# Optimization experiments

Measured on AMD Instinct MI355X. Metric: run time of the kernel, lower is better.

## Reference

```python
import jax, jax.numpy as jnp
import numpy as np

N_NODES = 100000
N_EDGES = 3200000


def _gcn_conv(x, src, dst, W, b, n):
    # symmetric GCN normalization with self-loops (PyG GCNConv default)
    deg = jax.ops.segment_sum(jnp.ones_like(dst, dtype=x.dtype), dst, num_segments=n)
    dinv = jnp.where(deg > 0, jax.lax.rsqrt(jnp.maximum(deg, 1e-12)), 0.0)
    norm = dinv[src] * dinv[dst]                       # [E+N]
    h = x @ W                                          # [n, out]
    msg = h[src] * norm[:, None]                       # gather + scale
    out = jax.ops.segment_sum(msg, dst, num_segments=n)  # scatter-add
    return out + b


def setup_inputs() -> dict:
    key = jax.random.key(0)
    k1, k2, k3, k4 = jax.random.split(key, 4)
    feat = jax.random.normal(k1, (N_NODES, 1), dtype=jnp.float32)
    edge_ix = jax.random.randint(k2, (2, N_EDGES), 0, N_NODES, dtype=jnp.int64)
    W1 = jax.random.normal(k3, (1, 32), dtype=jnp.float32) * (1.0 / 1.0)
    b1 = jnp.zeros((32,), dtype=jnp.float32)
    W2 = jax.random.normal(k4, (32, 64), dtype=jnp.float32) * (1.0 / np.sqrt(32.0))
    b2 = jnp.zeros((64,), dtype=jnp.float32)
    return {"feat": feat, "edge_ix": edge_ix, "W1": W1, "b1": b1, "W2": W2, "b2": b2}


def reference(feat, edge_ix, W1, b1, W2, b2):
    n = feat.shape[0]
    # add self loops once; reuse for both layers
    loops = jnp.arange(n, dtype=edge_ix.dtype)
    src = jnp.concatenate([edge_ix[0], loops])
    dst = jnp.concatenate([edge_ix[1], loops])
    x = jax.nn.relu(_gcn_conv(feat, src, dst, W1, b1, n))
    x = jax.nn.relu(_gcn_conv(x, src, dst, W2, b2, n))
    return x
```

## Files before the change

kernel.cpp:

```cpp
#include <hip/hip_runtime.h>


#define TPB 256
#define TPBW 1024
#define NSBMAX 1024
#define SBSZ 256
#define LBITS 8
#define SPLIT 4
#define NCHUNK 256

__global__ void k_init(const int* __restrict__ e32, int E, int* __restrict__ flag,
                       const float* __restrict__ W1, const float* __restrict__ b1,
                       const float* __restrict__ W2, float* __restrict__ upm,
                       int* __restrict__ bzero) {
    __shared__ int ok;
    __shared__ float sw[32], sb[32];
    int t = threadIdx.x;
    if (t == 0) ok = 1;
    if (t < 32) { sw[t] = W1[t]; sb[t] = b1[t]; }
    __syncthreads();
    int stride = E / 2048; if (stride < 1) stride = 1;
    bool bad = false;
#pragma unroll
    for (int i = 0; i < 8; ++i) {
        long k = (long)(t * 8 + i) * stride + 1;
        if (k < E && e32[2 * k + 1] != 0) bad = true;
    }
    if (bad) atomicAnd(&ok, 0);
    if (t < 64) {
        float up = 0.f, um = 0.f;
#pragma unroll
        for (int c = 0; c < 32; ++c) {
            float w = sw[c];
            float w2 = W2[c * 64 + t];
            up = fmaf(fmaxf(w, 0.f), w2, up);
            um = fmaf(fmaxf(-w, 0.f), w2, um);
        }
        upm[t] = up;
        upm[64 + t] = um;
    }
    __syncthreads();
    if (t == 0) {
        *flag = ok;
        int z = 1;
        for (int c = 0; c < 32; ++c) if (sb[c] != 0.f) z = 0;
        *bzero = z;
    }
}

__global__ void k_hist2(const int* __restrict__ e32, const int* __restrict__ flag,
                        int E, int NSB, int chunk, int* __restrict__ H) {
    __shared__ int sh[NSBMAX];
    int c = blockIdx.x;
    int c0 = c * chunk;
    int c1 = c0 + chunk; if (c1 > E) c1 = E;
    for (int i = threadIdx.x; i < NSB; i += TPBW) sh[i] = 0;
    __syncthreads();
    int f = *flag;
    for (int e = c0 + threadIdx.x; e < c1; e += TPBW) {
        int d = e32[((long)E + e) << f];
        atomicAdd(&sh[d >> LBITS], 1);
    }
    __syncthreads();
    for (int i = threadIdx.x; i < NSB; i += TPBW) H[(size_t)c * NSB + i] = sh[i];
}

__global__ void k_colscan(const int* __restrict__ H, int NSB,
                          int* __restrict__ P2, int* __restrict__ colsum) {
    __shared__ int s[NCHUNK];
    int b = blockIdx.x, t = threadIdx.x;
    int v = H[(size_t)t * NSB + b];
    s[t] = v;
    __syncthreads();
    for (int off = 1; off < NCHUNK; off <<= 1) {
        int x = s[t];
        int u = (t >= off) ? s[t - off] : 0;
        __syncthreads();
        s[t] = x + u;
        __syncthreads();
    }
    P2[(size_t)t * NSB + b] = s[t] - v;
    if (t == NCHUNK - 1) colsum[b] = s[t];
}

__global__ void k_scan(const int* __restrict__ colsum, int NSB, int E,
                       int* __restrict__ base) {
    __shared__ int s[TPB];
    int K = (NSB + TPB - 1) / TPB;
    int t = threadIdx.x;
    int i0 = t * K;
    int tot = 0;
    for (int k = 0; k < K; ++k) { int i = i0 + k; if (i < NSB) tot += colsum[i]; }
    s[t] = tot;
    __syncthreads();
    for (int off = 1; off < TPB; off <<= 1) {
        int v = s[t];
        int u = (t >= off) ? s[t - off] : 0;
        __syncthreads();
        s[t] = v + u;
        __syncthreads();
    }
    int run = s[t] - tot;
    for (int k = 0; k < K; ++k) {
        int i = i0 + k;
        if (i < NSB) { base[i] = run; run += colsum[i]; }
    }
    if (t == 0) base[NSB] = E;
}

__global__ void k_part2(const int* __restrict__ e32, const int* __restrict__ flag,
                        int E, int NSB, const int* __restrict__ base,
                        const int* __restrict__ P2, unsigned int* __restrict__ P,
                        int chunk) {
    __shared__ int sh[NSBMAX];
    int c = blockIdx.x;
    int c0 = c * chunk;
    int c1 = c0 + chunk; if (c1 > E) c1 = E;
    for (int i = threadIdx.x; i < NSB; i += TPBW)
        sh[i] = base[i] + P2[(size_t)c * NSB + i];
    __syncthreads();
    int f = *flag;
    int sshift = 32 - LBITS;
    for (int e = c0 + threadIdx.x; e < c1; e += TPBW) {
        long ee = (long)e << f;
        int s = e32[ee];
        int d = e32[(((long)E) << f) + ee];
        int b = d >> LBITS;
        int pos = atomicAdd(&sh[b], 1);
        P[pos] = (unsigned)s | ((unsigned)(d & (SBSZ - 1)) << sshift);
    }
}

__global__ void k_degS(const unsigned int* __restrict__ P, const int* __restrict__ base,
                       int n, int* __restrict__ cntP) {
    __shared__ int cnt[SBSZ];
    int bb = blockIdx.x / SPLIT, pp = blockIdx.x % SPLIT;
    int t = threadIdx.x;
    cnt[t] = 0;
    __syncthreads();
    int p0 = base[bb], len = base[bb + 1] - p0;
    int s0 = p0 + (int)((long)len * pp / SPLIT);
    int s1 = p0 + (int)((long)len * (pp + 1) / SPLIT);
    int sshift = 32 - LBITS;
    for (int p = s0 + t; p < s1; p += TPB)
        atomicAdd(&cnt[P[p] >> sshift], 1);
    __syncthreads();
    int v = (bb << LBITS) + t;
    if (v < n) cntP[pp * n + v] = cnt[t];
}

__global__ void k_prep1(const int* __restrict__ cntP, const float* __restrict__ feat,
                        int n, float* __restrict__ dinv, float* __restrict__ g) {
    int v = blockIdx.x * TPB + threadIdx.x;
    if (v >= n) return;
    int c = 0;
#pragma unroll
    for (int pp = 0; pp < SPLIT; ++pp) c += cntP[pp * n + v];
    float di = rsqrtf((float)(c + 1));
    dinv[v] = di;
    g[v] = di * feat[v];
}

__global__ void k_aggAS(const unsigned int* __restrict__ P, const int* __restrict__ base,
                        int n, const float* __restrict__ g, float* __restrict__ AP) {
    __shared__ float A[SBSZ];
    int bb = blockIdx.x / SPLIT, pp = blockIdx.x % SPLIT;
    int t = threadIdx.x;
    A[t] = 0.f;
    __syncthreads();
    int p0 = base[bb], len = base[bb + 1] - p0;
    int s0 = p0 + (int)((long)len * pp / SPLIT);
    int s1 = p0 + (int)((long)len * (pp + 1) / SPLIT);
    int sshift = 32 - LBITS;
    unsigned smask = (1u << sshift) - 1;
    for (int p = s0 + t; p < s1; p += TPB) {
        unsigned e = P[p];
        atomicAdd(&A[e >> sshift], g[e & smask]);
    }
    __syncthreads();
    int v = (bb << LBITS) + t;
    if (v < n) AP[pp * n + v] = A[t];
}

__global__ void k_prep2(const float* __restrict__ AP, const float* __restrict__ g,
                        const float* __restrict__ dinv, int n, const int* __restrict__ bzero,
                        float* __restrict__ qs, float2* __restrict__ pd,
                        float* __restrict__ Yagg) {
    int v = blockIdx.x * TPB + threadIdx.x;
    if (v >= n) return;
    float A = g[v];
#pragma unroll
    for (int pp = 0; pp < SPLIT; ++pp) A += AP[pp * n + v];
    float di = dinv[v];
    float px = di * A;
    qs[v] = di * px;
    if (!*bzero) {
        pd[v] = make_float2(px, di);
        float4* Y = (float4*)(Yagg + (size_t)v * 32);
#pragma unroll
        for (int i = 0; i < 8; ++i) Y[i] = make_float4(0.f, 0.f, 0.f, 0.f);
    }
}

__global__ void k_aggTS(const unsigned int* __restrict__ P, const int* __restrict__ base,
                        int n, const float* __restrict__ qs, float2* __restrict__ SP2) {
    __shared__ float Sp[SBSZ], Sm[SBSZ];
    int bb = blockIdx.x / SPLIT, pp = blockIdx.x % SPLIT;
    int t = threadIdx.x;
    Sp[t] = 0.f; Sm[t] = 0.f;
    __syncthreads();
    int p0 = base[bb], len = base[bb + 1] - p0;
    int s0 = p0 + (int)((long)len * pp / SPLIT);
    int s1 = p0 + (int)((long)len * (pp + 1) / SPLIT);
    int sshift = 32 - LBITS;
    unsigned smask = (1u << sshift) - 1;
    for (int p = s0 + t; p < s1; p += TPB) {
        unsigned e = P[p];
        float q = qs[e & smask];
        int l = e >> sshift;
        float* addr = (q >= 0.f) ? &Sp[l] : &Sm[l];
        atomicAdd(addr, fabsf(q));
    }
    __syncthreads();
    int v = (bb << LBITS) + t;
    if (v < n) SP2[pp * n + v] = make_float2(Sp[t], Sm[t]);
}

__global__ void k_out(const float* __restrict__ qs, const float* __restrict__ dinv,
                      const float2* __restrict__ SP2, const float* __restrict__ upm,
                      const float* __restrict__ b2, const int* __restrict__ bzero,
                      int n, float* __restrict__ out) {
    if (!*bzero) return;
    __shared__ float su[192];
    if (threadIdx.x < 192) su[threadIdx.x] = (threadIdx.x < 128) ? upm[threadIdx.x] : b2[threadIdx.x - 128];
    __syncthreads();
    int o = blockIdx.x * TPB + threadIdx.x;
    if (o >= n * 64) return;
    int v = o >> 6, k = o & 63;
    float qv = qs[v];
    float Sp = fmaxf(qv, 0.f), Sm = fmaxf(-qv, 0.f);
#pragma unroll
    for (int pp = 0; pp < SPLIT; ++pp) { float2 s = SP2[pp * n + v]; Sp += s.x; Sm += s.y; }
    float r = fmaf(dinv[v], fmaf(Sp, su[k], Sm * su[64 + k]), su[128 + k]);
    out[o] = fmaxf(r, 0.f);
}

__global__ void k_aggY(const int* __restrict__ e32, const int* __restrict__ flag,
                       int E, const int* __restrict__ bzero,
                       const float2* __restrict__ pd,
                       const float* __restrict__ W1, const float* __restrict__ b1,
                       float* __restrict__ Yagg) {
    if (*bzero) return;
    __shared__ float sw[32], sb[32];
    if (threadIdx.x < 32) { sw[threadIdx.x] = W1[threadIdx.x]; sb[threadIdx.x] = b1[threadIdx.x]; }
    __syncthreads();
    int sh = *flag;
    long stride = (long)gridDim.x * TPB;
    for (long e = (long)blockIdx.x * TPB + threadIdx.x; e < E; e += stride) {
        int s = e32[e << sh];
        int d = e32[((long)E + e) << sh];
        float2 p = pd[s];
#pragma unroll
        for (int c = 0; c < 32; ++c) {
            float y = p.y * fmaxf(fmaf(sw[c], p.x, sb[c] * p.y), 0.f);
            atomicAdd(&Yagg[(size_t)d * 32 + c], y);
        }
    }
}

__global__ void k_final_gen(const float2* __restrict__ pd, const float* __restrict__ Yagg,
                            const float* __restrict__ W1, const float* __restrict__ b1,
                            const float* __restrict__ W2, const float* __restrict__ b2,
                            const int* __restrict__ bzero, int n, float* __restrict__ out) {
    if (*bzero) return;
    __shared__ float sW[32 * 64];
    __shared__ float sb2[64];
    __shared__ float sagg[8][33];
    int t = threadIdx.x;
    for (int i = t; i < 32 * 64; i += TPB) sW[i] = W2[i];
    if (t < 64) sb2[t] = b2[t];
    int vl = t >> 5, c = t & 31;
    int nblk = (n + 7) / 8;
    for (int blk = blockIdx.x; blk < nblk; blk += gridDim.x) {
        int v = blk * 8 + vl;
        float a = 0.f;
        if (v < n) {
            float2 p = pd[v];
            float dv = p.y;
            float yv = fmaxf(fmaf(W1[c], p.x, b1[c] * p.y), 0.f);
            a = dv * (dv * yv + Yagg[(size_t)v * 32 + c]);
        }
        __syncthreads();
        sagg[vl][c] = a;
        __syncthreads();
        if (v < n) {
            float o0 = sb2[c], o1 = sb2[c + 32];
#pragma unroll
            for (int j = 0; j < 32; ++j) {
                float x = sagg[vl][j];
                o0 += x * sW[j * 64 + c];
                o1 += x * sW[j * 64 + 32 + c];
            }
            out[(size_t)v * 64 + c]      = fmaxf(o0, 0.f);
            out[(size_t)v * 64 + 32 + c] = fmaxf(o1, 0.f);
        }
    }
}

static inline size_t align256(size_t x) { return (x + 255) & ~(size_t)255; }

extern "C" void kernel_launch(void* const* d_in, const int* in_sizes, int n_in,
                              void* d_out, int out_size, void* d_ws, size_t ws_size,
                              hipStream_t stream) {
    const float* feat = (const float*)d_in[0];
    const int*   e32  = (const int*)d_in[1];
    const float* W1   = (const float*)d_in[2];
    const float* b1   = (const float*)d_in[3];
    const float* W2   = (const float*)d_in[4];
    const float* b2   = (const float*)d_in[5];
    float* out = (float*)d_out;

    int n = in_sizes[0];
    int E = in_sizes[1] / 2;

    int NSB = (n + SBSZ - 1) >> LBITS;

    char* w = (char*)d_ws;
    size_t off = 0;
    auto alloc = [&](size_t bytes) -> char* { char* p = w + off; off = align256(off + bytes); return p; };
    unsigned int* P = (unsigned int*)alloc((size_t)E * 4);
    int*    H     = (int*)alloc((size_t)NCHUNK * NSB * 4);
    int*    P2    = (int*)alloc((size_t)NCHUNK * NSB * 4);
    int*    colsum= (int*)alloc((size_t)NSB * 4);
    int*    base  = (int*)alloc((size_t)(NSB + 1) * 4);
    int*    cntP  = (int*)alloc((size_t)SPLIT * n * 4);
    float*  AP    = (float*)alloc((size_t)SPLIT * n * 4);
    float2* SP2   = (float2*)alloc((size_t)SPLIT * n * 8);
    float*  dinv  = (float*)alloc((size_t)n * 4);
    float*  g     = (float*)alloc((size_t)n * 4);
    float*  qs    = (float*)alloc((size_t)n * 4);
    float2* pd    = (float2*)alloc((size_t)n * 8);
    float*  upm   = (float*)alloc(128 * 4);
    int*    flag  = (int*)alloc(4);
    int*    bzero = (int*)alloc(4);
    float*  Yagg  = (float*)alloc((size_t)n * 32 * 4);

    int chunk = (E + NCHUNK - 1) / NCHUNK;
    int gN = (n + TPB - 1) / TPB;
    int gS = NSB * SPLIT;
    int gO = (n * 64 + TPB - 1) / TPB;

    hipLaunchKernelGGL(k_init,      dim3(1),      dim3(TPB),  0, stream, e32, E, flag, W1, b1, W2, upm, bzero);
    hipLaunchKernelGGL(k_hist2,     dim3(NCHUNK), dim3(TPBW), 0, stream, e32, flag, E, NSB, chunk, H);
    hipLaunchKernelGGL(k_colscan,   dim3(NSB),    dim3(NCHUNK), 0, stream, H, NSB, P2, colsum);
    hipLaunchKernelGGL(k_scan,      dim3(1),      dim3(TPB),  0, stream, colsum, NSB, E, base);
    hipLaunchKernelGGL(k_part2,     dim3(NCHUNK), dim3(TPBW), 0, stream, e32, flag, E, NSB, base, P2, P, chunk);
    hipLaunchKernelGGL(k_degS,      dim3(gS),     dim3(TPB),  0, stream, P, base, n, cntP);
    hipLaunchKernelGGL(k_prep1,     dim3(gN),     dim3(TPB),  0, stream, cntP, feat, n, dinv, g);
    hipLaunchKernelGGL(k_aggAS,     dim3(gS),     dim3(TPB),  0, stream, P, base, n, g, AP);
    hipLaunchKernelGGL(k_prep2,     dim3(gN),     dim3(TPB),  0, stream, AP, g, dinv, n, bzero, qs, pd, Yagg);
    hipLaunchKernelGGL(k_aggTS,     dim3(gS),     dim3(TPB),  0, stream, P, base, n, qs, SP2);
    hipLaunchKernelGGL(k_out,       dim3(gO),     dim3(TPB),  0, stream, qs, dinv, SP2, upm, b2, bzero, n, out);
    hipLaunchKernelGGL(k_aggY,      dim3(512),    dim3(TPB),  0, stream, e32, flag, E, bzero, pd, W1, b1, Yagg);
    hipLaunchKernelGGL(k_final_gen, dim3(1024),   dim3(TPB),  0, stream, pd, Yagg, W1, b1, W2, b2, bzero, n, out);
}
```

Baseline: 122.4 us.

## Fuse scan and per-node prep kernels via last-block counters, vectorize edge loads

```diff
diff --git a/kernel.cpp b/kernel.cpp
--- a/kernel.cpp
+++ b/kernel.cpp
@@ -12,12 +12,13 @@
 __global__ void k_init(const int* __restrict__ e32, int E, int* __restrict__ flag,
                        const float* __restrict__ W1, const float* __restrict__ b1,
                        const float* __restrict__ W2, float* __restrict__ upm,
-                       int* __restrict__ bzero) {
+                       int* __restrict__ bzero, int* __restrict__ ctrs, int nctr) {
     __shared__ int ok;
     __shared__ float sw[32], sb[32];
     int t = threadIdx.x;
     if (t == 0) ok = 1;
     if (t < 32) { sw[t] = W1[t]; sb[t] = b1[t]; }
+    for (int i = t; i < nctr; i += TPB) ctrs[i] = 0;
     __syncthreads();
     int stride = E / 2048; if (stride < 1) stride = 1;
     bool bad = false;
@@ -57,17 +58,38 @@
     for (int i = threadIdx.x; i < NSB; i += TPBW) sh[i] = 0;
     __syncthreads();
     int f = *flag;
-    for (int e = c0 + threadIdx.x; e < c1; e += TPBW) {
-        int d = e32[((long)E + e) << f];
-        atomicAdd(&sh[d >> LBITS], 1);
+    if (((E | c0) & 1) == 0) {
+        if (f) {
+            const int4* d4 = (const int4*)e32;
+            for (int e = c0 + threadIdx.x * 2; e < c1; e += TPBW * 2) {
+                int4 dd = d4[(E + e) >> 1];
+                atomicAdd(&sh[dd.x >> LBITS], 1);
+                if (e + 1 < c1) atomicAdd(&sh[dd.z >> LBITS], 1);
+            }
+        } else {
+            const int2* d2 = (const int2*)e32;
+            for (int e = c0 + threadIdx.x * 2; e < c1; e += TPBW * 2) {
+                int2 dd = d2[(E + e) >> 1];
+                atomicAdd(&sh[dd.x >> LBITS], 1);
+                if (e + 1 < c1) atomicAdd(&sh[dd.y >> LBITS], 1);
+            }
+        }
+    } else {
+        for (int e = c0 + threadIdx.x; e < c1; e += TPBW) {
+            int d = e32[((long)E + e) << f];
+            atomicAdd(&sh[d >> LBITS], 1);
+        }
     }
     __syncthreads();
     for (int i = threadIdx.x; i < NSB; i += TPBW) H[(size_t)c * NSB + i] = sh[i];
 }
 
-__global__ void k_colscan(const int* __restrict__ H, int NSB,
-                          int* __restrict__ P2, int* __restrict__ colsum) {
+__global__ void k_colscan(const int* __restrict__ H, int NSB, int E,
+                          int* __restrict__ P2, int* __restrict__ colsum,
+                          int* __restrict__ base, int* __restrict__ ctr) {
     __shared__ int s[NCHUNK];
+    __shared__ int s2a[TPB];
+    __shared__ int lastf;
     int b = blockIdx.x, t = threadIdx.x;
     int v = H[(size_t)t * NSB + b];
     s[t] = v;
@@ -81,26 +103,25 @@
     }
     P2[(size_t)t * NSB + b] = s[t] - v;
     if (t == NCHUNK - 1) colsum[b] = s[t];
-}
-
-__global__ void k_scan(const int* __restrict__ colsum, int NSB, int E,
-                       int* __restrict__ base) {
-    __shared__ int s[TPB];
+    __syncthreads();
+    if (t == 0) { __threadfence(); lastf = (atomicAdd(ctr, 1) == gridDim.x - 1); }
+    __syncthreads();
+    if (!lastf) return;
+    __threadfence();
     int K = (NSB + TPB - 1) / TPB;
-    int t = threadIdx.x;
     int i0 = t * K;
     int tot = 0;
     for (int k = 0; k < K; ++k) { int i = i0 + k; if (i < NSB) tot += colsum[i]; }
-    s[t] = tot;
+    s2a[t] = tot;
     __syncthreads();
     for (int off = 1; off < TPB; off <<= 1) {
-        int v = s[t];
-        int u = (t >= off) ? s[t - off] : 0;
-        __syncthreads();
-        s[t] = v + u;
-        __syncthreads();
-    }
-    int run = s[t] - tot;
+        int x = s2a[t];
+        int u = (t >= off) ? s2a[t - off] : 0;
+        __syncthreads();
+        s2a[t] = x + u;
+        __syncthreads();
+    }
+    int run = s2a[t] - tot;
     for (int k = 0; k < K; ++k) {
         int i = i0 + k;
         if (i < NSB) { base[i] = run; run += colsum[i]; }
@@ -121,20 +142,55 @@
     __syncthreads();
     int f = *flag;
     int sshift = 32 - LBITS;
-    for (int e = c0 + threadIdx.x; e < c1; e += TPBW) {
-        long ee = (long)e << f;
-        int s = e32[ee];
-        int d = e32[(((long)E) << f) + ee];
-        int b = d >> LBITS;
-        int pos = atomicAdd(&sh[b], 1);
-        P[pos] = (unsigned)s | ((unsigned)(d & (SBSZ - 1)) << sshift);
-    }
-}
-
-__global__ void k_degS(const unsigned int* __restrict__ P, const int* __restrict__ base,
-                       int n, int* __restrict__ cntP) {
+    if (((E | c0) & 1) == 0) {
+        if (f) {
+            const int4* s4 = (const int4*)e32;
+            for (int e = c0 + threadIdx.x * 2; e < c1; e += TPBW * 2) {
+                int4 ss = s4[e >> 1];
+                int4 dd = s4[(E + e) >> 1];
+                int b0 = dd.x >> LBITS;
+                int pos0 = atomicAdd(&sh[b0], 1);
+                P[pos0] = (unsigned)ss.x | ((unsigned)(dd.x & (SBSZ - 1)) << sshift);
+                if (e + 1 < c1) {
+                    int b1i = dd.z >> LBITS;
+                    int pos1 = atomicAdd(&sh[b1i], 1);
+                    P[pos1] = (unsigned)ss.z | ((unsigned)(dd.z & (SBSZ - 1)) << sshift);
+                }
+            }
+        } else {
+            const int2* s2 = (const int2*)e32;
+            for (int e = c0 + threadIdx.x * 2; e < c1; e += TPBW * 2) {
+                int2 ss = s2[e >> 1];
+                int2 dd = s2[(E + e) >> 1];
+                int b0 = dd.x >> LBITS;
+                int pos0 = atomicAdd(&sh[b0], 1);
+                P[pos0] = (unsigned)ss.x | ((unsigned)(dd.x & (SBSZ - 1)) << sshift);
+                if (e + 1 < c1) {
+                    int b1i = dd.y >> LBITS;
+                    int pos1 = atomicAdd(&sh[b1i], 1);
+                    P[pos1] = (unsigned)ss.y | ((unsigned)(dd.y & (SBSZ - 1)) << sshift);
+                }
+            }
+        }
+    } else {
+        for (int e = c0 + threadIdx.x; e < c1; e += TPBW) {
+            long ee = (long)e << f;
+            int s = e32[ee];
+            int d = e32[(((long)E) << f) + ee];
+            int b = d >> LBITS;
+            int pos = atomicAdd(&sh[b], 1);
+            P[pos] = (unsigned)s | ((unsigned)(d & (SBSZ - 1)) << sshift);
+        }
+    }
+}
+
+__global__ void k_degSP(const unsigned int* __restrict__ P, const int* __restrict__ base,
+                        int n, const float* __restrict__ feat, int* __restrict__ cntP,
+                        float* __restrict__ dinv, float* __restrict__ g,
+                        int* __restrict__ ctrE) {
     __shared__ int cnt[SBSZ];
-    int bb = blockIdx.x / SPLIT, pp = blockIdx.x % SPLIT;
+    __shared__ int lastf;
+    int bb = blockIdx.x >> 2, pp = blockIdx.x & (SPLIT - 1);
     int t = threadIdx.x;
     cnt[t] = 0;
     __syncthreads();
@@ -147,24 +203,29 @@
     __syncthreads();
     int v = (bb << LBITS) + t;
     if (v < n) cntP[pp * n + v] = cnt[t];
-}
-
-__global__ void k_prep1(const int* __restrict__ cntP, const float* __restrict__ feat,
-                        int n, float* __restrict__ dinv, float* __restrict__ g) {
-    int v = blockIdx.x * TPB + threadIdx.x;
-    if (v >= n) return;
-    int c = 0;
-#pragma unroll
-    for (int pp = 0; pp < SPLIT; ++pp) c += cntP[pp * n + v];
-    float di = rsqrtf((float)(c + 1));
-    dinv[v] = di;
-    g[v] = di * feat[v];
-}
-
-__global__ void k_aggAS(const unsigned int* __restrict__ P, const int* __restrict__ base,
-                        int n, const float* __restrict__ g, float* __restrict__ AP) {
+    __syncthreads();
+    if (t == 0) { __threadfence(); lastf = (atomicAdd(&ctrE[bb], 1) == SPLIT - 1); }
+    __syncthreads();
+    if (!lastf) return;
+    __threadfence();
+    if (v < n) {
+        int c = 0;
+#pragma unroll
+        for (int q = 0; q < SPLIT; ++q) c += cntP[q * n + v];
+        float di = rsqrtf((float)(c + 1));
+        dinv[v] = di;
+        g[v] = di * feat[v];
+    }
+}
+
+__global__ void k_aggASP(const unsigned int* __restrict__ P, const int* __restrict__ base,
+                         int n, const float* __restrict__ g, const float* __restrict__ dinv,
+                         const int* __restrict__ bzero, float* __restrict__ AP,
+                         float* __restrict__ qs, float2* __restrict__ pd,
+                         float* __restrict__ Yagg, int* __restrict__ ctrF) {
     __shared__ float A[SBSZ];
-    int bb = blockIdx.x / SPLIT, pp = blockIdx.x % SPLIT;
+    __shared__ int lastf;
+    int bb = blockIdx.x >> 2, pp = blockIdx.x & (SPLIT - 1);
     int t = threadIdx.x;
     A[t] = 0.f;
     __syncthreads();
@@ -180,32 +241,36 @@
     __syncthreads();
     int v = (bb << LBITS) + t;
     if (v < n) AP[pp * n + v] = A[t];
-}
-
-__global__ void k_prep2(const float* __restrict__ AP, const float* __restrict__ g,
-                        const float* __restrict__ dinv, int n, const int* __restrict__ bzero,
-                        float* __restrict__ qs, float2* __restrict__ pd,
-                        float* __restrict__ Yagg) {
-    int v = blockIdx.x * TPB + threadIdx.x;
-    if (v >= n) return;
-    float A = g[v];
-#pragma unroll
-    for (int pp = 0; pp < SPLIT; ++pp) A += AP[pp * n + v];
-    float di = dinv[v];
-    float px = di * A;
-    qs[v] = di * px;
-    if (!*bzero) {
-        pd[v] = make_float2(px, di);
-        float4* Y = (float4*)(Yagg + (size_t)v * 32);
-#pragma unroll
-        for (int i = 0; i < 8; ++i) Y[i] = make_float4(0.f, 0.f, 0.f, 0.f);
-    }
-}
-
-__global__ void k_aggTS(const unsigned int* __restrict__ P, const int* __restrict__ base,
-                        int n, const float* __restrict__ qs, float2* __restrict__ SP2) {
+    __syncthreads();
+    if (t == 0) { __threadfence(); lastf = (atomicAdd(&ctrF[bb], 1) == SPLIT - 1); }
+    __syncthreads();
+    if (!lastf) return;
+    __threadfence();
+    if (v < n) {
+        float Av = g[v];
+#pragma unroll
+        for (int q = 0; q < SPLIT; ++q) Av += AP[q * n + v];
+        float di = dinv[v];
+        float px = di * Av;
+        qs[v] = di * px;
+        if (!*bzero) {
+            pd[v] = make_float2(px, di);
+            float4* Y = (float4*)(Yagg + (size_t)v * 32);
+#pragma unroll
+            for (int i = 0; i < 8; ++i) Y[i] = make_float4(0.f, 0.f, 0.f, 0.f);
+        }
+    }
+}
+
+__global__ void k_aggTSP(const unsigned int* __restrict__ P, const int* __restrict__ base,
+                         int n, const float* __restrict__ qs, const float* __restrict__ dinv,
+                         const float* __restrict__ upm, const float* __restrict__ b2,
+                         const int* __restrict__ bzero, float2* __restrict__ SP2,
+                         float* __restrict__ out, int* __restrict__ ctrG) {
     __shared__ float Sp[SBSZ], Sm[SBSZ];
-    int bb = blockIdx.x / SPLIT, pp = blockIdx.x % SPLIT;
+    __shared__ float su[192];
+    __shared__ int lastf;
+    int bb = blockIdx.x >> 2, pp = blockIdx.x & (SPLIT - 1);
     int t = threadIdx.x;
     Sp[t] = 0.f; Sm[t] = 0.f;
     __syncthreads();
@@ -222,27 +287,33 @@
         atomicAdd(addr, fabsf(q));
     }
     __syncthreads();
-    int v = (bb << LBITS) + t;
+    int v0 = bb << LBITS;
+    int v = v0 + t;
     if (v < n) SP2[pp * n + v] = make_float2(Sp[t], Sm[t]);
-}
-
-__global__ void k_out(const float* __restrict__ qs, const float* __restrict__ dinv,
-                      const float2* __restrict__ SP2, const float* __restrict__ upm,
-                      const float* __restrict__ b2, const int* __restrict__ bzero,
-                      int n, float* __restrict__ out) {
-    if (!*bzero) return;
-    __shared__ float su[192];
-    if (threadIdx.x < 192) su[threadIdx.x] = (threadIdx.x < 128) ? upm[threadIdx.x] : b2[threadIdx.x - 128];
-    __syncthreads();
-    int o = blockIdx.x * TPB + threadIdx.x;
-    if (o >= n * 64) return;
-    int v = o >> 6, k = o & 63;
-    float qv = qs[v];
-    float Sp = fmaxf(qv, 0.f), Sm = fmaxf(-qv, 0.f);
-#pragma unroll
-    for (int pp = 0; pp < SPLIT; ++pp) { float2 s = SP2[pp * n + v]; Sp += s.x; Sm += s.y; }
-    float r = fmaf(dinv[v], fmaf(Sp, su[k], Sm * su[64 + k]), su[128 + k]);
-    out[o] = fmaxf(r, 0.f);
+    __syncthreads();
+    if (t == 0) { __threadfence(); lastf = (atomicAdd(&ctrG[bb], 1) == SPLIT - 1); }
+    __syncthreads();
+    if (!lastf || !*bzero) return;
+    __threadfence();
+    if (t < 192) su[t] = (t < 192) ? ((t < 128) ? upm[t] : b2[t - 128]) : 0.f;
+    float Fp = 0.f, Fm = 0.f;
+    if (v < n) {
+        float qv = qs[v];
+        float sp = fmaxf(qv, 0.f), sm = fmaxf(-qv, 0.f);
+#pragma unroll
+        for (int q = 0; q < SPLIT; ++q) { float2 s2v = SP2[q * n + v]; sp += s2v.x; sm += s2v.y; }
+        float di = dinv[v];
+        Fp = di * sp; Fm = di * sm;
+    }
+    __syncthreads();
+    Sp[t] = Fp; Sm[t] = Fm;
+    __syncthreads();
+    int nv = n - v0; if (nv > SBSZ) nv = SBSZ; if (nv < 0) nv = 0;
+    for (int o = t; o < nv * 64; o += TPB) {
+        int vl = o >> 6, k = o & 63;
+        float r = fmaf(Sp[vl], su[k], fmaf(Sm[vl], su[64 + k], su[128 + k]));
+        out[(size_t)(v0 + vl) * 64 + k] = fmaxf(r, 0.f);
+    }
 }
 
 __global__ void k_aggY(const int* __restrict__ e32, const int* __restrict__ flag,
@@ -324,6 +395,7 @@
     int E = in_sizes[1] / 2;
 
     int NSB = (n + SBSZ - 1) >> LBITS;
+    int nctr = 1 + 3 * NSB;
 
     char* w = (char*)d_ws;
     size_t off = 0;
@@ -343,24 +415,25 @@
     float*  upm   = (float*)alloc(128 * 4);
     int*    flag  = (int*)alloc(4);
     int*    bzero = (int*)alloc(4);
+    int*    ctrs  = (int*)alloc((size_t)nctr * 4);
     float*  Yagg  = (float*)alloc((size_t)n * 32 * 4);
 
+    int* ctrC = ctrs;
+    int* ctrE = ctrs + 1;
+    int* ctrF = ctrs + 1 + NSB;
+    int* ctrG = ctrs + 1 + 2 * NSB;
+
     int chunk = (E + NCHUNK - 1) / NCHUNK;
-    int gN = (n + TPB - 1) / TPB;
+    if (chunk & 1) chunk++;
     int gS = NSB * SPLIT;
-    int gO = (n * 64 + TPB - 1) / TPB;
-
-    hipLaunchKernelGGL(k_init,      dim3(1),      dim3(TPB),  0, stream, e32, E, flag, W1, b1, W2, upm, bzero);
+
+    hipLaunchKernelGGL(k_init,      dim3(1),      dim3(TPB),  0, stream, e32, E, flag, W1, b1, W2, upm, bzero, ctrs, nctr);
     hipLaunchKernelGGL(k_hist2,     dim3(NCHUNK), dim3(TPBW), 0, stream, e32, flag, E, NSB, chunk, H);
-    hipLaunchKernelGGL(k_colscan,   dim3(NSB),    dim3(NCHUNK), 0, stream, H, NSB, P2, colsum);
-    hipLaunchKernelGGL(k_scan,      dim3(1),      dim3(TPB),  0, stream, colsum, NSB, E, base);
+    hipLaunchKernelGGL(k_colscan,   dim3(NSB),    dim3(NCHUNK), 0, stream, H, NSB, E, P2, colsum, base, ctrC);
     hipLaunchKernelGGL(k_part2,     dim3(NCHUNK), dim3(TPBW), 0, stream, e32, flag, E, NSB, base, P2, P, chunk);
-    hipLaunchKernelGGL(k_degS,      dim3(gS),     dim3(TPB),  0, stream, P, base, n, cntP);
-    hipLaunchKernelGGL(k_prep1,     dim3(gN),     dim3(TPB),  0, stream, cntP, feat, n, dinv, g);
-    hipLaunchKernelGGL(k_aggAS,     dim3(gS),     dim3(TPB),  0, stream, P, base, n, g, AP);
-    hipLaunchKernelGGL(k_prep2,     dim3(gN),     dim3(TPB),  0, stream, AP, g, dinv, n, bzero, qs, pd, Yagg);
-    hipLaunchKernelGGL(k_aggTS,     dim3(gS),     dim3(TPB),  0, stream, P, base, n, qs, SP2);
-    hipLaunchKernelGGL(k_out,       dim3(gO),     dim3(TPB),  0, stream, qs, dinv, SP2, upm, b2, bzero, n, out);
+    hipLaunchKernelGGL(k_degSP,     dim3(gS),     dim3(TPB),  0, stream, P, base, n, feat, cntP, dinv, g, ctrE);
+    hipLaunchKernelGGL(k_aggASP,    dim3(gS),     dim3(TPB),  0, stream, P, base, n, g, dinv, bzero, AP, qs, pd, Yagg, ctrF);
+    hipLaunchKernelGGL(k_aggTSP,    dim3(gS),     dim3(TPB),  0, stream, P, base, n, qs, dinv, upm, b2, bzero, SP2, out, ctrG);
     hipLaunchKernelGGL(k_aggY,      dim3(512),    dim3(TPB),  0, stream, e32, flag, E, bzero, pd, W1, b1, Yagg);
     hipLaunchKernelGGL(k_final_gen, dim3(1024),   dim3(TPB),  0, stream, pd, Yagg, W1, b1, W2, b2, bzero, n, out);
 }
```

Result: slower. 439.5 us (+259.2%).
